# Kernel tuning notes

Measured on AMD Instinct MI355X. Metric: run time of the kernel, lower is better.

The kernel has to match this reference:

```python
import jax, jax.numpy as jnp
import numpy as np

NUM_SAMPLES = 64
NUM_FINE_SAMPLES = 128
BATCH = 131072


def setup_inputs() -> dict:
    key = jax.random.key(0)
    k1, k2, k3, k4 = jax.random.split(key, 4)
    near = 0.5 + jax.random.uniform(k1, (BATCH, 1), dtype=jnp.float32)          # [0.5, 1.5]
    far = near + 2.0 + 4.0 * jax.random.uniform(k2, (BATCH, 1), dtype=jnp.float32)  # near + [2, 6]
    density = 5.0 * jax.random.uniform(k3, (BATCH, NUM_SAMPLES), dtype=jnp.float32)
    rgb = jax.random.uniform(k4, (BATCH, NUM_SAMPLES, 3), dtype=jnp.float32)
    return {"near": near, "far": far, "density": density, "rgb": rgb}


def _hierarchical_sample(bins, weights, num_samples):
    # bins, weights: [B, N]; deterministic u (pertube=False branch)
    B, N = weights.shape
    pdf = weights / (jnp.sum(weights, -1, keepdims=True) + 1e-6)
    cdf = jnp.cumsum(pdf, -1)                                   # [B, N]
    u = jnp.broadcast_to(jnp.linspace(0.05, 0.95, num_samples, dtype=bins.dtype), (B, num_samples))
    inds = jax.vmap(lambda c, uu: jnp.searchsorted(c, uu, side='right'))(cdf, u)  # [B, Nf]
    below = jnp.maximum(inds - 1, 0)
    above = jnp.minimum(inds, N - 1)
    cdf_b = jnp.take_along_axis(cdf, below, -1)
    cdf_a = jnp.take_along_axis(cdf, above, -1)
    bins_b = jnp.take_along_axis(bins, below, -1)
    bins_a = jnp.take_along_axis(bins, above, -1)
    denom = cdf_a - cdf_b
    denom = jnp.where(denom < 1e-5, jnp.ones_like(denom), denom)
    t = (u - cdf_b) / denom
    return bins_b + t * (bins_a - bins_b)                       # [B, Nf]


def reference(near, far, density, rgb):
    # --- coarse frustum (deterministic, pertub=False path of _sample_coarse_frustum) ---
    unit = jnp.linspace(0.0, 1.0, NUM_SAMPLES + 1, dtype=near.dtype)  # [N+1]
    zs_edges = near * (1.0 - unit) + far * unit                 # [B, N+1]
    start, end = zs_edges[:, :-1], zs_edges[:, 1:]
    deltas = end - start                                        # [B, N]
    mids = 0.5 * (start + end)                                  # frustum.zs, [B, N]

    # --- _compute_weight: alpha compositing transmittance ---
    alpha = 1.0 - jnp.exp(-density * deltas)                    # [B, N]
    trans = jnp.cumprod(jnp.concatenate([jnp.ones_like(alpha[:, :1]), 1.0 - alpha], -1), -1)[:, :-1]
    weight = alpha * trans                                      # [B, N]

    # --- _sample_fine_frustum: inverse-CDF sampling + merge-sort of zs ---
    fine_zs = _hierarchical_sample(mids, weight, NUM_FINE_SAMPLES)  # [B, Nf] (no_grad in original)
    fine_zs = jax.lax.stop_gradient(fine_zs)
    combined_zs = jnp.sort(jnp.concatenate([mids, fine_zs], -1), -1)  # [B, N+Nf]

    # --- volume_render of the coarse pass ---
    rgb_out = jnp.sum(weight[..., None] * rgb, axis=1)          # [B, 3]
    acc = jnp.sum(weight, -1, keepdims=True)                    # [B, 1]
    depth = jnp.sum(weight * mids, -1, keepdims=True) / (acc + 1e-8)  # normalized composite
    return combined_zs, rgb_out, depth, acc
```

## Files before the change

### kernel.cpp

```cpp
#include <hip/hip_runtime.h>

#define BATCH 131072
#define NS 64
#define NF 128
#define NTOT 192
#define WAVES_PER_BLOCK 4

__global__ __launch_bounds__(256) void pdf_sampler_kernel(
    const float* __restrict__ near_p,
    const float* __restrict__ far_p,
    const float* __restrict__ density,
    const float* __restrict__ rgb,
    float* __restrict__ out)
{
    const int lane = threadIdx.x & 63;
    const int wave = threadIdx.x >> 6;
    const int ray  = blockIdx.x * WAVES_PER_BLOCK + wave;

    __shared__ float s_cdf [WAVES_PER_BLOCK][NS];
    __shared__ float s_mids[WAVES_PER_BLOCK][NS];
    __shared__ float s_fine[WAVES_PER_BLOCK][NF];
    __shared__ float s_comb[WAVES_PER_BLOCK][NTOT];

    const float nearv = near_p[ray];
    const float farv  = far_p[ray];

    const float u0 = (float)lane       * (1.0f / 64.0f);
    const float u1 = (float)(lane + 1) * (1.0f / 64.0f);
    const float zs = nearv * (1.0f - u0) + farv * u0;
    const float ze = nearv * (1.0f - u1) + farv * u1;
    const float delta = ze - zs;
    const float mid   = 0.5f * (zs + ze);

    const float dens  = density[ray * NS + lane];
    const float alpha = 1.0f - expf(-dens * delta);

    float p = 1.0f - alpha;
    #pragma unroll
    for (int off = 1; off < 64; off <<= 1) {
        float t = __shfl_up(p, off, 64);
        if (lane >= off) p *= t;
    }
    float trans = __shfl_up(p, 1, 64);
    if (lane == 0) trans = 1.0f;
    const float w = alpha * trans;

    float wsum = w;
    #pragma unroll
    for (int off = 32; off; off >>= 1) wsum += __shfl_xor(wsum, off, 64);

    float cdfv = w / (wsum + 1e-6f);
    #pragma unroll
    for (int off = 1; off < 64; off <<= 1) {
        float t = __shfl_up(cdfv, off, 64);
        if (lane >= off) cdfv += t;
    }
    s_cdf [wave][lane] = cdfv;
    s_mids[wave][lane] = mid;

    const float r = rgb[(ray * NS + lane) * 3 + 0];
    const float g = rgb[(ray * NS + lane) * 3 + 1];
    const float b = rgb[(ray * NS + lane) * 3 + 2];
    float wr = w * r, wg = w * g, wb = w * b, wm = w * mid;
    #pragma unroll
    for (int off = 32; off; off >>= 1) {
        wr += __shfl_xor(wr, off, 64);
        wg += __shfl_xor(wg, off, 64);
        wb += __shfl_xor(wb, off, 64);
        wm += __shfl_xor(wm, off, 64);
    }
    if (lane == 0) {
        float* rgb_out   = out + (size_t)BATCH * NTOT;
        float* depth_out = rgb_out + (size_t)BATCH * 3;
        float* acc_out   = depth_out + BATCH;
        rgb_out[ray * 3 + 0] = wr;
        rgb_out[ray * 3 + 1] = wg;
        rgb_out[ray * 3 + 2] = wb;
        depth_out[ray] = wm / (wsum + 1e-8f);
        acc_out[ray]   = wsum;
    }

    __syncthreads();

    const float* cdf  = s_cdf[wave];
    const float* mids = s_mids[wave];
    #pragma unroll
    for (int k = lane; k < NF; k += 64) {
        const float u = 0.05f + (0.9f / 127.0f) * (float)k;
        int lo = 0, hi = NS;
        while (lo < hi) {
            int m = (lo + hi) >> 1;
            if (cdf[m] <= u) lo = m + 1; else hi = m;
        }
        const int inds  = lo;
        const int below = inds > 0 ? inds - 1 : 0;
        const int above = inds < NS - 1 ? inds : NS - 1;
        const float cb = cdf[below], ca = cdf[above];
        const float bb = mids[below], ba = mids[above];
        float denom = ca - cb;
        if (denom < 1e-5f) denom = 1.0f;
        const float t = (u - cb) / denom;
        s_fine[wave][k] = bb + t * (ba - bb);
    }

    __syncthreads();

    const float* fine = s_fine[wave];
    {
        int lo = 0, hi = NF;
        while (lo < hi) {
            int m = (lo + hi) >> 1;
            if (fine[m] < mid) lo = m + 1; else hi = m;
        }
        s_comb[wave][lane + lo] = mid;
    }
    #pragma unroll
    for (int k = lane; k < NF; k += 64) {
        const float f = fine[k];
        int lo = 0, hi = NS;
        while (lo < hi) {
            int m = (lo + hi) >> 1;
            if (mids[m] <= f) lo = m + 1; else hi = m;
        }
        s_comb[wave][k + lo] = f;
    }

    __syncthreads();

    float* comb_out = out + (size_t)ray * NTOT;
    if (lane < 48) {
        const float* src = &s_comb[wave][lane * 4];
        float4 v = make_float4(src[0], src[1], src[2], src[3]);
        reinterpret_cast<float4*>(comb_out)[lane] = v;
    }
}

extern "C" void kernel_launch(void* const* d_in, const int* in_sizes, int n_in,
                              void* d_out, int out_size, void* d_ws, size_t ws_size,
                              hipStream_t stream) {
    const float* near_p  = (const float*)d_in[0];
    const float* far_p   = (const float*)d_in[1];
    const float* density = (const float*)d_in[2];
    const float* rgb     = (const float*)d_in[3];
    float* out = (float*)d_out;

    const int grid = BATCH / WAVES_PER_BLOCK;
    pdf_sampler_kernel<<<grid, 256, 0, stream>>>(near_p, far_p, density, rgb, out);
}
```

Measured before the change: 247.1 us.

## Replace binary searches with scatter-based inverse CDF and closed-form merge positions

```diff
diff --git a/kernel.cpp b/kernel.cpp
--- a/kernel.cpp
+++ b/kernel.cpp
@@ -4,7 +4,7 @@
 #define NS 64
 #define NF 128
 #define NTOT 192
-#define WAVES_PER_BLOCK 4
+#define WPB 4
 
 __global__ __launch_bounds__(256) void pdf_sampler_kernel(
     const float* __restrict__ near_p,
@@ -15,12 +15,11 @@
 {
     const int lane = threadIdx.x & 63;
     const int wave = threadIdx.x >> 6;
-    const int ray  = blockIdx.x * WAVES_PER_BLOCK + wave;
+    const int ray  = blockIdx.x * WPB + wave;
 
-    __shared__ float s_cdf [WAVES_PER_BLOCK][NS];
-    __shared__ float s_mids[WAVES_PER_BLOCK][NS];
-    __shared__ float s_fine[WAVES_PER_BLOCK][NF];
-    __shared__ float s_comb[WAVES_PER_BLOCK][NTOT];
+    __shared__ float2 s_cm  [WPB][NS];
+    __shared__ int    s_inds[WPB][NF];
+    __shared__ __align__(16) float s_comb[WPB][NTOT];
 
     const float nearv = near_p[ray];
     const float farv  = far_p[ray];
@@ -32,31 +31,36 @@
     const float delta = ze - zs;
     const float mid   = 0.5f * (zs + ze);
 
-    const float dens  = density[ray * NS + lane];
-    const float alpha = 1.0f - expf(-dens * delta);
+    const float dens = density[ray * NS + lane];
 
-    float p = 1.0f - alpha;
+    float S = dens * delta;
     #pragma unroll
     for (int off = 1; off < 64; off <<= 1) {
-        float t = __shfl_up(p, off, 64);
-        if (lane >= off) p *= t;
+        float t = __shfl_up(S, off, 64);
+        if (lane >= off) S += t;
     }
-    float trans = __shfl_up(p, 1, 64);
-    if (lane == 0) trans = 1.0f;
-    const float w = alpha * trans;
+    const float e = expf(-S);
+    float eprev = __shfl_up(e, 1, 64);
+    if (lane == 0) eprev = 1.0f;
+    const float w = eprev - e;
 
-    float wsum = w;
-    #pragma unroll
-    for (int off = 32; off; off >>= 1) wsum += __shfl_xor(wsum, off, 64);
+    const float wsum = 1.0f - __shfl(e, 63, 64);
+    const float cdfv = (1.0f - e) * __builtin_amdgcn_rcpf(wsum + 1e-6f);
 
-    float cdfv = w / (wsum + 1e-6f);
-    #pragma unroll
-    for (int off = 1; off < 64; off <<= 1) {
-        float t = __shfl_up(cdfv, off, 64);
-        if (lane >= off) cdfv += t;
-    }
-    s_cdf [wave][lane] = cdfv;
-    s_mids[wave][lane] = mid;
+    s_cm[wave][lane] = make_float2(cdfv, mid);
+
+    const float step = 0.9f / 127.0f;
+    int t = (int)ceilf((cdfv - 0.05f) * (127.0f / 0.9f));
+    t = t < 0 ? 0 : (t > 128 ? 128 : t);
+    while (t > 0   && __fmaf_rn(step, (float)(t - 1), 0.05f) >= cdfv) --t;
+    while (t < 128 && __fmaf_rn(step, (float)t,       0.05f) <  cdfv) ++t;
+
+    int t1 = __shfl_down(t, 1, 64);
+    if (lane == 63) t1 = 128;
+    const int t0 = __shfl(t, 0, 64);
+
+    for (int k = lane; k < t0; k += 64) s_inds[wave][k] = 0;
+    for (int k = t; k < t1; ++k) s_inds[wave][k] = lane + 1;
 
     const float r = rgb[(ray * NS + lane) * 3 + 0];
     const float g = rgb[(ray * NS + lane) * 3 + 1];
@@ -82,55 +86,29 @@
 
     __syncthreads();
 
-    const float* cdf  = s_cdf[wave];
-    const float* mids = s_mids[wave];
     #pragma unroll
-    for (int k = lane; k < NF; k += 64) {
-        const float u = 0.05f + (0.9f / 127.0f) * (float)k;
-        int lo = 0, hi = NS;
-        while (lo < hi) {
-            int m = (lo + hi) >> 1;
-            if (cdf[m] <= u) lo = m + 1; else hi = m;
-        }
-        const int inds  = lo;
+    for (int i = 0; i < 2; ++i) {
+        const int k = lane + 64 * i;
+        const int inds  = s_inds[wave][k];
         const int below = inds > 0 ? inds - 1 : 0;
-        const int above = inds < NS - 1 ? inds : NS - 1;
-        const float cb = cdf[below], ca = cdf[above];
-        const float bb = mids[below], ba = mids[above];
-        float denom = ca - cb;
+        const int above = inds < 63 ? inds : 63;
+        const float2 cb2 = s_cm[wave][below];
+        const float2 ca2 = s_cm[wave][above];
+        float denom = ca2.x - cb2.x;
         if (denom < 1e-5f) denom = 1.0f;
-        const float t = (u - cb) / denom;
-        s_fine[wave][k] = bb + t * (ba - bb);
+        const float u  = __fmaf_rn(step, (float)k, 0.05f);
+        const float tt = (u - cb2.x) * __builtin_amdgcn_rcpf(denom);
+        const float fine = cb2.y + tt * (ca2.y - cb2.y);
+        s_comb[wave][k + below + 1] = fine;
     }
-
-    __syncthreads();
-
-    const float* fine = s_fine[wave];
-    {
-        int lo = 0, hi = NF;
-        while (lo < hi) {
-            int m = (lo + hi) >> 1;
-            if (fine[m] < mid) lo = m + 1; else hi = m;
-        }
-        s_comb[wave][lane + lo] = mid;
-    }
-    #pragma unroll
-    for (int k = lane; k < NF; k += 64) {
-        const float f = fine[k];
-        int lo = 0, hi = NS;
-        while (lo < hi) {
-            int m = (lo + hi) >> 1;
-            if (mids[m] <= f) lo = m + 1; else hi = m;
-        }
-        s_comb[wave][k + lo] = f;
-    }
+    const int pm = (lane == 0) ? 0 : lane + t;
+    s_comb[wave][pm] = mid;
 
     __syncthreads();
 
     float* comb_out = out + (size_t)ray * NTOT;
     if (lane < 48) {
-        const float* src = &s_comb[wave][lane * 4];
-        float4 v = make_float4(src[0], src[1], src[2], src[3]);
+        const float4 v = *reinterpret_cast<const float4*>(&s_comb[wave][lane * 4]);
         reinterpret_cast<float4*>(comb_out)[lane] = v;
     }
 }
@@ -144,6 +122,6 @@
     const float* rgb     = (const float*)d_in[3];
     float* out = (float*)d_out;
 
-    const int grid = BATCH / WAVES_PER_BLOCK;
+    const int grid = BATCH / WPB;
     pdf_sampler_kernel<<<grid, 256, 0, stream>>>(near_p, far_p, density, rgb, out);
 }
```

Measured after the change: 235.7 us. 4.6% less time.
